# Performance work log

Measured on AMD Instinct MI355X. Metric: run time of the kernel, lower is better.

## Reference

```python
import jax, jax.numpy as jnp
import numpy as np
import math

IN_FEATURES = 256
OUT_FEATURES = 128
B, N = 4, 4096


def setup_inputs() -> dict:
    key = jax.random.key(0)
    ks = jax.random.split(key, 8)
    h = jax.random.normal(ks[0], (B, N, IN_FEATURES), dtype=jnp.float32)
    adj = jax.random.randint(ks[1], (B, N, N), 0, 2, dtype=jnp.int32)
    # Linear params (torch nn.Linear: y = x @ W.T + b)
    s = 1.0 / math.sqrt(IN_FEATURES)
    Wq = jax.random.uniform(ks[2], (OUT_FEATURES, IN_FEATURES), jnp.float32, -s, s)
    bq = jax.random.uniform(ks[3], (OUT_FEATURES,), jnp.float32, -s, s)
    Wk = jax.random.uniform(ks[4], (OUT_FEATURES, IN_FEATURES), jnp.float32, -s, s)
    bk = jax.random.uniform(ks[5], (OUT_FEATURES,), jnp.float32, -s, s)
    Wv = jax.random.uniform(ks[6], (OUT_FEATURES, IN_FEATURES), jnp.float32, -s, s)
    bv = jax.random.uniform(ks[7], (OUT_FEATURES,), jnp.float32, -s, s)
    return {"h": h, "adj": adj, "Wq": Wq, "bq": bq, "Wk": Wk, "bk": bk, "Wv": Wv, "bv": bv}


def reference(h, adj, Wq, bq, Wk, bk, Wv, bv):
    # QKV projections: [B, N, D]
    q = jnp.einsum('bnf,df->bnd', h, Wq) + bq
    k = jnp.einsum('bnf,df->bnd', h, Wk) + bk
    v = jnp.einsum('bnf,df->bnd', h, Wv) + bv
    # Dense scores [B, N, N], scaled
    scores = jnp.einsum('bnd,bmd->bnm', q, k) / math.sqrt(OUT_FEATURES)
    neg = jnp.float32(-9e15)
    scores = jnp.where(adj > 0, scores, neg)
    probs = jax.nn.softmax(scores, axis=-1)
    return jnp.einsum('bnm,bmd->bnd', probs, v)
```

## Files before the change

kernel.cpp:

```cpp
#include <hip/hip_runtime.h>
#include <stdint.h>
#include <math.h>

#define NB 4
#define NN 4096
#define NF 256
#define ND 128
#define KVB 32
#define NR (NB * NN)
#define QKVE ((size_t)NR * ND)

typedef __bf16 bf16x8 __attribute__((ext_vector_type(8)));
typedef __bf16 bf16x4v __attribute__((ext_vector_type(4)));
typedef float f32x4 __attribute__((ext_vector_type(4)));
typedef unsigned short u16x4 __attribute__((ext_vector_type(4)));

__device__ __forceinline__ unsigned short f2bf(float f) {
    union { float f; uint32_t u; } v; v.f = f;
    uint32_t r = (v.u + 0x7FFFu + ((v.u >> 16) & 1u)) >> 16;
    return (unsigned short)r;
}
__device__ __forceinline__ bf16x8 lds_read16(const unsigned short* base, int byte_off) {
    return *reinterpret_cast<const bf16x8*>(reinterpret_cast<const char*>(base) + byte_off);
}
__device__ __forceinline__ void gld_lds16(const void* g, void* l) {
    __builtin_amdgcn_global_load_lds(
        (const __attribute__((address_space(1))) void*)g,
        (__attribute__((address_space(3))) void*)l, 16, 0, 0);
}

__global__ __launch_bounds__(256) void pack_proj(
    const int* __restrict__ adj, unsigned long long* __restrict__ pm64,
    const float* __restrict__ h,
    const float* __restrict__ Wq, const float* __restrict__ bq,
    const float* __restrict__ Wk, const float* __restrict__ bk,
    const float* __restrict__ Wv, const float* __restrict__ bv,
    unsigned short* __restrict__ qo, unsigned short* __restrict__ ko,
    unsigned short* __restrict__ vs, float qscale)
{
    __shared__ unsigned short h_lds[64 * 128];
    __shared__ unsigned short w_lds[128 * 128];

    const int tid = threadIdx.x;
    const int lane = tid & 63;

    if (blockIdx.x < 1024) {
        const int w = tid >> 6;
        const size_t base = ((size_t)blockIdx.x * 4 + w) * 256;
        for (int o = 0; o < 32; ++o) {
            const size_t wb = base + o * 8;
            int v[8];
#pragma unroll
            for (int u = 0; u < 8; ++u)
                v[u] = adj[(wb + u) * 64 + lane];
            unsigned long long m[8];
#pragma unroll
            for (int u = 0; u < 8; ++u)
                m[u] = __ballot(v[u] != 0);
            if (lane == 0) {
#pragma unroll
                for (int u = 0; u < 8; u += 2) {
                    ulonglong2 st; st.x = m[u]; st.y = m[u + 1];
                    *reinterpret_cast<ulonglong2*>(pm64 + wb + u) = st;
                }
            }
        }
        return;
    }

    const int idx = blockIdx.x - 1024;
    const int proj = idx >> 8;
    const int R0 = (idx & 255) * 64;
    const int wv = tid >> 6;
    const int l15 = lane & 15;
    const int lhi = lane >> 4;

    const float* W    = proj == 0 ? Wq : (proj == 1 ? Wk : Wv);
    const float* bias = proj == 0 ? bq : (proj == 1 ? bk : bv);
    const float scale = proj == 0 ? qscale : 1.0f;

    f32x4 acc[8];
#pragma unroll
    for (int i = 0; i < 8; ++i) acc[i] = f32x4{0.f, 0.f, 0.f, 0.f};

    for (int kc = 0; kc < 2; ++kc) {
        const int c0 = kc * 128;
        __syncthreads();
#pragma unroll
        for (int p = 0; p < 8; ++p) {
            int i2 = p * 256 + tid;
            int row = i2 >> 5;
            int seg = i2 & 31;
            f32x4 hv = *reinterpret_cast<const f32x4*>(h + (size_t)(R0 + row) * NF + c0 + seg * 4);
            u16x4 hb;
            hb[0] = f2bf(hv[0]); hb[1] = f2bf(hv[1]); hb[2] = f2bf(hv[2]); hb[3] = f2bf(hv[3]);
            int byte = (row * 256 + seg * 8) ^ ((row & 7) << 4);
            *reinterpret_cast<u16x4*>(reinterpret_cast<char*>(h_lds) + byte) = hb;
        }
#pragma unroll
        for (int p = 0; p < 16; ++p) {
            int i2 = p * 256 + tid;
            int row = i2 >> 5;
            int seg = i2 & 31;
            f32x4 wv4 = *reinterpret_cast<const f32x4*>(W + (size_t)row * NF + c0 + seg * 4);
            u16x4 wb;
            wb[0] = f2bf(wv4[0]); wb[1] = f2bf(wv4[1]); wb[2] = f2bf(wv4[2]); wb[3] = f2bf(wv4[3]);
            int byte = (row * 256 + seg * 8) ^ ((row & 7) << 4);
            *reinterpret_cast<u16x4*>(reinterpret_cast<char*>(w_lds) + byte) = wb;
        }
        __syncthreads();
        const int arow = 16 * wv + l15;
#pragma unroll
        for (int ks = 0; ks < 4; ++ks) {
            int k = ks * 32 + 8 * lhi;
            bf16x8 a = lds_read16(h_lds, (arow * 256 + k * 2) ^ ((arow & 7) << 4));
#pragma unroll
            for (int cs = 0; cs < 8; ++cs) {
                int d = 16 * cs + l15;
                bf16x8 b = lds_read16(w_lds, (d * 256 + k * 2) ^ ((d & 7) << 4));
                acc[cs] = __builtin_amdgcn_mfma_f32_16x16x32_bf16(a, b, acc[cs], 0, 0, 0);
            }
        }
    }
    if (proj < 2) {
        unsigned short* out = proj == 0 ? qo : ko;
#pragma unroll
        for (int cs = 0; cs < 8; ++cs) {
            int d = 16 * cs + l15;
            float bb = bias[d];
#pragma unroll
            for (int j = 0; j < 4; ++j) {
                int row = R0 + 16 * wv + 4 * lhi + j;
                out[(size_t)row * ND + d] = f2bf((acc[cs][j] + bb) * scale);
            }
        }
    } else {
        const int bb_ = R0 >> 12;
        const int nb_ = (R0 & (NN - 1)) + 16 * wv + 4 * lhi;
        const int pt = nb_ >> 5;
        const int ch = (nb_ >> 3) & 3;
        const int mm0 = nb_ & 7;
#pragma unroll
        for (int cs = 0; cs < 8; ++cs) {
            int d = 16 * cs + l15;
            float bb = bias[d];
            u16x4 o;
#pragma unroll
            for (int j = 0; j < 4; ++j) o[j] = f2bf(acc[cs][j] + bb);
            size_t oidx = ((size_t)(bb_ * 128 + pt)) * 4096 + ch * 1024 + d * 8 + mm0;
            *reinterpret_cast<u16x4*>(vs + oidx) = o;
        }
    }
}

__global__ __launch_bounds__(256, 2) void attn(
    const unsigned short* __restrict__ Q,
    const unsigned short* __restrict__ K,
    const unsigned short* __restrict__ VS,
    const unsigned int* __restrict__ pm,
    float* __restrict__ out,
    float* __restrict__ opart1,
    float* __restrict__ ml,
    int ntl)
{
    __shared__ unsigned short stA[8192];
    __shared__ unsigned short stB[8192];
    __shared__ unsigned short p_lds[4096];

    const int tid = threadIdx.x;
    const int lane = tid & 63;
    const int w = tid >> 6;
    const int l15 = lane & 15;
    const int lhi = lane >> 4;

    const int flat = blockIdx.x;
    const int x = flat & 7;
    const int rest = flat >> 3;
    const int qt = rest & 31;
    const int s2 = rest >> 5;
    const int combo = x + 8 * s2;
    const int b = combo & 3;
    const int sp = combo >> 2;
    const int q0w = qt * 128 + w * 32;
    const size_t bN = (size_t)b * NN;
    const int ptbase = sp * ntl;

    const unsigned short* Kb = K + bN * ND;
    const unsigned short* Vbase = VS + (size_t)b * 128 * 4096;

    bf16x8 qf[2][4];
#pragma unroll
    for (int g = 0; g < 2; ++g)
#pragma unroll
        for (int ks = 0; ks < 4; ++ks)
            qf[g][ks] = *reinterpret_cast<const bf16x8*>(
                Q + (bN + q0w + g * 16 + l15) * ND + ks * 32 + 8 * lhi);

    const unsigned int* pmr0 = pm + (bN + (size_t)(q0w + l15)) * 128;
    const unsigned int* pmr1 = pm + (bN + (size_t)(q0w + 16 + l15)) * 128;

    f32x4 acc[2][8];
#pragma unroll
    for (int g = 0; g < 2; ++g)
#pragma unroll
        for (int i = 0; i < 8; ++i) acc[g][i] = f32x4{0.f, 0.f, 0.f, 0.f};
    float m_run[2] = {-INFINITY, -INFINITY};
    float l_part[2] = {0.f, 0.f};

    auto stage = [&](unsigned short* st, int pt) {
        const int m0 = pt * KVB;
#pragma unroll
        for (int i = 0; i < 4; ++i) {
            int c = w * 4 + i;
            if (c < 8) {
                int ms = c >> 2, ks = c & 3;
                const unsigned short* src = Kb
                    + (size_t)(m0 + ms * 16 + l15) * ND + ks * 32 + lhi * 8;
                gld_lds16(src, st + c * 512);
            } else {
                int vi = c - 8;
                const unsigned short* src = Vbase + (size_t)pt * 4096 + vi * 512 + lane * 8;
                gld_lds16(src, st + 4096 + vi * 512);
            }
        }
    };

    auto compute = [&](const unsigned short* st, unsigned int mw0, unsigned int mw1) {
        bf16x8 kf[2][4];
#pragma unroll
        for (int ms = 0; ms < 2; ++ms)
#pragma unroll
            for (int ks = 0; ks < 4; ++ks)
                kf[ms][ks] = lds_read16(st, (ms * 4 + ks) * 1024 + lane * 16);

        f32x4 s[2][2];
#pragma unroll
        for (int g = 0; g < 2; ++g)
#pragma unroll
            for (int ms = 0; ms < 2; ++ms) s[g][ms] = f32x4{0.f, 0.f, 0.f, 0.f};
        __builtin_amdgcn_s_setprio(1);
#pragma unroll
        for (int g = 0; g < 2; ++g)
#pragma unroll
            for (int ms = 0; ms < 2; ++ms)
#pragma unroll
                for (int ks = 0; ks < 4; ++ks)
                    s[g][ms] = __builtin_amdgcn_mfma_f32_16x16x32_bf16(
                        kf[ms][ks], qf[g][ks], s[g][ms], 0, 0, 0);
        __builtin_amdgcn_s_setprio(0);

        bf16x8 vf[8];
#pragma unroll
        for (int ds = 0; ds < 8; ++ds)
            vf[ds] = lds_read16(st + 4096, lhi * 2048 + ds * 256 + l15 * 16);

        const unsigned int mw[2] = {mw0, mw1};
        float smaxl[2];
        float dmax = -INFINITY;
#pragma unroll
        for (int g = 0; g < 2; ++g) {
            unsigned int mwg = mw[g] >> (4 * lhi);
#pragma unroll
            for (int ms = 0; ms < 2; ++ms)
#pragma unroll
                for (int r = 0; r < 4; ++r)
                    if (!((mwg >> (16 * ms + r)) & 1u)) s[g][ms][r] = -1.0e30f;
            float mx = fmaxf(fmaxf(fmaxf(s[g][0][0], s[g][0][1]), fmaxf(s[g][0][2], s[g][0][3])),
                             fmaxf(fmaxf(s[g][1][0], s[g][1][1]), fmaxf(s[g][1][2], s[g][1][3])));
            smaxl[g] = mx;
            dmax = fmaxf(dmax, mx - m_run[g]);
        }
        if (!__all(dmax <= 8.0f)) {
#pragma unroll
            for (int g = 0; g < 2; ++g) {
                float mx = smaxl[g];
                mx = fmaxf(mx, __shfl_xor(mx, 16, 64));
                mx = fmaxf(mx, __shfl_xor(mx, 32, 64));
                float mnew = fmaxf(m_run[g], mx);
                float c = exp2f(m_run[g] - mnew);
                m_run[g] = mnew;
                l_part[g] *= c;
#pragma unroll
                for (int ds = 0; ds < 8; ++ds) acc[g][ds] *= c;
            }
        }

#pragma unroll
        for (int g = 0; g < 2; ++g) {
            bf16x4v pbv[2];
#pragma unroll
            for (int ms = 0; ms < 2; ++ms)
#pragma unroll
                for (int r = 0; r < 4; ++r) {
                    float p = exp2f(s[g][ms][r] - m_run[g]);
                    __bf16 pb = (__bf16)p;
                    l_part[g] += (float)pb;
                    pbv[ms][r] = pb;
                }
            const int base = (w * 2 + g) * 1024 + l15 * 64;
#pragma unroll
            for (int ms = 0; ms < 2; ++ms)
                *reinterpret_cast<bf16x4v*>(reinterpret_cast<char*>(p_lds)
                    + base + ms * 32 + lhi * 8) = pbv[ms];
            bf16x8 pa = lds_read16(p_lds, base + lhi * 16);
            __builtin_amdgcn_s_setprio(1);
#pragma unroll
            for (int ds = 0; ds < 8; ++ds)
                acc[g][ds] = __builtin_amdgcn_mfma_f32_16x16x32_bf16(
                    vf[ds], pa, acc[g][ds], 0, 0, 0);
            __builtin_amdgcn_s_setprio(0);
        }
    };

    stage(stA, ptbase);
    __syncthreads();

    uint4 mk[2], mk2[2];
    mk[0] = *reinterpret_cast<const uint4*>(pmr0 + ptbase);
    mk[1] = *reinterpret_cast<const uint4*>(pmr1 + ptbase);
    for (int t = 0; t < ntl; t += 4) {
        int tn4 = (t + 4 < ntl) ? t + 4 : t;
        mk2[0] = *reinterpret_cast<const uint4*>(pmr0 + ptbase + tn4);
        mk2[1] = *reinterpret_cast<const uint4*>(pmr1 + ptbase + tn4);

        stage(stB, ptbase + t + 1);
        compute(stA, mk[0].x, mk[1].x);
        __syncthreads();
        stage(stA, ptbase + t + 2 < ptbase + ntl ? ptbase + t + 2 : ptbase + ntl - 1);
        compute(stB, mk[0].y, mk[1].y);
        __syncthreads();
        stage(stB, ptbase + t + 3 < ptbase + ntl ? ptbase + t + 3 : ptbase + ntl - 1);
        compute(stA, mk[0].z, mk[1].z);
        __syncthreads();
        stage(stA, ptbase + (t + 4 < ntl ? t + 4 : ntl - 1));
        compute(stB, mk[0].w, mk[1].w);
        __syncthreads();

        mk[0] = mk2[0]; mk[1] = mk2[1];
    }

#pragma unroll
    for (int g = 0; g < 2; ++g) {
        float rs = l_part[g];
        rs += __shfl_xor(rs, 16, 64);
        rs += __shfl_xor(rs, 32, 64);
        l_part[g] = rs;
    }

    float* op = (sp == 0) ? out : (opart1 + (size_t)(sp - 1) * NR * ND);
#pragma unroll
    for (int g = 0; g < 2; ++g) {
        const size_t rowbase = (bN + q0w + g * 16 + l15) * ND;
#pragma unroll
        for (int ds = 0; ds < 8; ++ds)
            *reinterpret_cast<f32x4*>(op + rowbase + 16 * ds + 4 * lhi) = acc[g][ds];
    }
    if (lhi == 0) {
#pragma unroll
        for (int g = 0; g < 2; ++g) {
            size_t gr = bN + q0w + g * 16 + l15;
            *reinterpret_cast<float2*>(ml + ((size_t)sp * NR + gr) * 2) =
                make_float2(m_run[g], l_part[g]);
        }
    }
}

__global__ __launch_bounds__(256) void merge_splits(
    float* __restrict__ out, const float* __restrict__ opart1,
    const float* __restrict__ ml, int nsplit)
{
    int idx = blockIdx.x * 256 + threadIdx.x;
    int row = idx >> 5;
    int d4 = (idx & 31) * 4;
    float mmax = ml[(size_t)row * 2];
    for (int sp = 1; sp < nsplit; ++sp)
        mmax = fmaxf(mmax, ml[((size_t)sp * NR + row) * 2]);
    f32x4 o0 = *reinterpret_cast<const f32x4*>(out + (size_t)row * ND + d4);
    float w0 = exp2f(ml[(size_t)row * 2] - mmax);
    float lsum = ml[(size_t)row * 2 + 1] * w0;
    f32x4 acc;
#pragma unroll
    for (int j = 0; j < 4; ++j) acc[j] = o0[j] * w0;
    for (int sp = 1; sp < nsplit; ++sp) {
        float m_s = ml[((size_t)sp * NR + row) * 2];
        float l_s = ml[((size_t)sp * NR + row) * 2 + 1];
        float ws_ = exp2f(m_s - mmax);
        f32x4 os = *reinterpret_cast<const f32x4*>(opart1 + ((size_t)(sp - 1) * NR + row) * ND + d4);
#pragma unroll
        for (int j = 0; j < 4; ++j) acc[j] += os[j] * ws_;
        lsum += l_s * ws_;
    }
    float inv = 1.0f / lsum;
    f32x4 r;
#pragma unroll
    for (int j = 0; j < 4; ++j) r[j] = acc[j] * inv;
    *reinterpret_cast<f32x4*>(out + (size_t)row * ND + d4) = r;
}

extern "C" void kernel_launch(void* const* d_in, const int* in_sizes, int n_in,
                              void* d_out, int out_size, void* d_ws, size_t ws_size,
                              hipStream_t stream) {
    const float* h  = (const float*)d_in[0];
    const int* adj  = (const int*)d_in[1];
    const float* Wq = (const float*)d_in[2];
    const float* bq = (const float*)d_in[3];
    const float* Wk = (const float*)d_in[4];
    const float* bk = (const float*)d_in[5];
    const float* Wv = (const float*)d_in[6];
    const float* bv = (const float*)d_in[7];
    float* out = (float*)d_out;

    unsigned short* qws  = (unsigned short*)d_ws;
    unsigned short* kws  = qws + QKVE;
    unsigned short* vsws = kws + QKVE;
    float* opart1 = (float*)(vsws + QKVE);

    const size_t pm_bytes = (size_t)NB * NN * (NN / 8);
    const size_t need4 = 3 * QKVE * 2 + 3 * QKVE * 4 + 4 * (size_t)NR * 2 * 4 + pm_bytes;
    const int nsplit = (ws_size >= need4) ? 4 : 2;
    float* mlws = opart1 + (size_t)(nsplit - 1) * NR * ND;
    unsigned int* pmws = (unsigned int*)(mlws + (size_t)nsplit * NR * 2);
    const int ntl = (NN / KVB) / nsplit;

    const float qscale = (float)(0.08838834764831845 / 0.6931471805599453);

    pack_proj<<<dim3(1024 + 768), 256, 0, stream>>>(
        adj, (unsigned long long*)pmws,
        h, Wq, bq, Wk, bk, Wv, bv, qws, kws, vsws, qscale);
    attn<<<dim3(32 * 4 * nsplit), 256, 0, stream>>>(
        qws, kws, vsws, pmws, out, opart1, mlws, ntl);
    merge_splits<<<dim3(NR * 32 / 256), 256, 0, stream>>>(out, opart1, mlws, nsplit);
}
```

Measured before the change: 152.8 us.

## Read int32 adjacency directly in attention instead of pre-packing bitmask

Removes the separate adjacency bit-packing pass from the projection kernel. The attention kernel now loads int32 adjacency values per tile straight from global memory, double-buffered alongside the K/V staging. This drops one full read of the 256MB adjacency plus the packed-mask write and re-read. In exchange the attention kernel reads 32x more mask bytes per tile inside its main loop, which may make it memory-bound.

Measured after the change: 124.6 us (median of 2 runs). -18.5%, faster.

```diff
diff --git a/kernel.cpp b/kernel.cpp
--- a/kernel.cpp
+++ b/kernel.cpp
@@ -13,6 +13,7 @@
 typedef __bf16 bf16x8 __attribute__((ext_vector_type(8)));
 typedef __bf16 bf16x4v __attribute__((ext_vector_type(4)));
 typedef float f32x4 __attribute__((ext_vector_type(4)));
+typedef int i32x4 __attribute__((ext_vector_type(4)));
 typedef unsigned short u16x4 __attribute__((ext_vector_type(4)));
 
 __device__ __forceinline__ unsigned short f2bf(float f) {
@@ -29,8 +30,7 @@
         (__attribute__((address_space(3))) void*)l, 16, 0, 0);
 }
 
-__global__ __launch_bounds__(256) void pack_proj(
-    const int* __restrict__ adj, unsigned long long* __restrict__ pm64,
+__global__ __launch_bounds__(256) void qkv_proj(
     const float* __restrict__ h,
     const float* __restrict__ Wq, const float* __restrict__ bq,
     const float* __restrict__ Wk, const float* __restrict__ bk,
@@ -43,34 +43,8 @@
 
     const int tid = threadIdx.x;
     const int lane = tid & 63;
-
-    if (blockIdx.x < 1024) {
-        const int w = tid >> 6;
-        const size_t base = ((size_t)blockIdx.x * 4 + w) * 256;
-        for (int o = 0; o < 32; ++o) {
-            const size_t wb = base + o * 8;
-            int v[8];
-#pragma unroll
-            for (int u = 0; u < 8; ++u)
-                v[u] = adj[(wb + u) * 64 + lane];
-            unsigned long long m[8];
-#pragma unroll
-            for (int u = 0; u < 8; ++u)
-                m[u] = __ballot(v[u] != 0);
-            if (lane == 0) {
-#pragma unroll
-                for (int u = 0; u < 8; u += 2) {
-                    ulonglong2 st; st.x = m[u]; st.y = m[u + 1];
-                    *reinterpret_cast<ulonglong2*>(pm64 + wb + u) = st;
-                }
-            }
-        }
-        return;
-    }
-
-    const int idx = blockIdx.x - 1024;
-    const int proj = idx >> 8;
-    const int R0 = (idx & 255) * 64;
+    const int proj = blockIdx.x >> 8;
+    const int R0 = (blockIdx.x & 255) * 64;
     const int wv = tid >> 6;
     const int l15 = lane & 15;
     const int lhi = lane >> 4;
@@ -157,7 +131,7 @@
     const unsigned short* __restrict__ Q,
     const unsigned short* __restrict__ K,
     const unsigned short* __restrict__ VS,
-    const unsigned int* __restrict__ pm,
+    const int* __restrict__ adj,
     float* __restrict__ out,
     float* __restrict__ opart1,
     float* __restrict__ ml,
@@ -187,6 +161,7 @@
 
     const unsigned short* Kb = K + bN * ND;
     const unsigned short* Vbase = VS + (size_t)b * 128 * 4096;
+    const int* adjb = adj + (size_t)b * NN * NN + (size_t)(q0w + l15) * NN + 4 * lhi;
 
     bf16x8 qf[2][4];
 #pragma unroll
@@ -195,9 +170,6 @@
         for (int ks = 0; ks < 4; ++ks)
             qf[g][ks] = *reinterpret_cast<const bf16x8*>(
                 Q + (bN + q0w + g * 16 + l15) * ND + ks * 32 + 8 * lhi);
-
-    const unsigned int* pmr0 = pm + (bN + (size_t)(q0w + l15)) * 128;
-    const unsigned int* pmr1 = pm + (bN + (size_t)(q0w + 16 + l15)) * 128;
 
     f32x4 acc[2][8];
 #pragma unroll
@@ -224,8 +196,17 @@
             }
         }
     };
-
-    auto compute = [&](const unsigned short* st, unsigned int mw0, unsigned int mw1) {
+    auto adjld = [&](i32x4 (&ma)[2][2], int pt) {
+        const int m0 = pt * KVB;
+#pragma unroll
+        for (int g = 0; g < 2; ++g)
+#pragma unroll
+            for (int ms = 0; ms < 2; ++ms)
+                ma[g][ms] = *reinterpret_cast<const i32x4*>(
+                    adjb + (size_t)(g * 16) * NN + m0 + 16 * ms);
+    };
+
+    auto compute = [&](const unsigned short* st, const i32x4 (&ma)[2][2]) {
         bf16x8 kf[2][4];
 #pragma unroll
         for (int ms = 0; ms < 2; ++ms)
@@ -254,17 +235,15 @@
         for (int ds = 0; ds < 8; ++ds)
             vf[ds] = lds_read16(st + 4096, lhi * 2048 + ds * 256 + l15 * 16);
 
-        const unsigned int mw[2] = {mw0, mw1};
         float smaxl[2];
         float dmax = -INFINITY;
 #pragma unroll
         for (int g = 0; g < 2; ++g) {
-            unsigned int mwg = mw[g] >> (4 * lhi);
 #pragma unroll
             for (int ms = 0; ms < 2; ++ms)
 #pragma unroll
                 for (int r = 0; r < 4; ++r)
-                    if (!((mwg >> (16 * ms + r)) & 1u)) s[g][ms][r] = -1.0e30f;
+                    if (ma[g][ms][r] == 0) s[g][ms][r] = -1.0e30f;
             float mx = fmaxf(fmaxf(fmaxf(s[g][0][0], s[g][0][1]), fmaxf(s[g][0][2], s[g][0][3])),
                              fmaxf(fmaxf(s[g][1][0], s[g][1][1]), fmaxf(s[g][1][2], s[g][1][3])));
             smaxl[g] = mx;
@@ -312,31 +291,21 @@
         }
     };
 
+    i32x4 maskA[2][2], maskB[2][2];
     stage(stA, ptbase);
+    adjld(maskA, ptbase);
     __syncthreads();
 
-    uint4 mk[2], mk2[2];
-    mk[0] = *reinterpret_cast<const uint4*>(pmr0 + ptbase);
-    mk[1] = *reinterpret_cast<const uint4*>(pmr1 + ptbase);
-    for (int t = 0; t < ntl; t += 4) {
-        int tn4 = (t + 4 < ntl) ? t + 4 : t;
-        mk2[0] = *reinterpret_cast<const uint4*>(pmr0 + ptbase + tn4);
-        mk2[1] = *reinterpret_cast<const uint4*>(pmr1 + ptbase + tn4);
-
+    for (int t = 0; t < ntl; t += 2) {
         stage(stB, ptbase + t + 1);
-        compute(stA, mk[0].x, mk[1].x);
+        adjld(maskB, ptbase + t + 1);
+        compute(stA, maskA);
         __syncthreads();
-        stage(stA, ptbase + t + 2 < ptbase + ntl ? ptbase + t + 2 : ptbase + ntl - 1);
-        compute(stB, mk[0].y, mk[1].y);
+        int t2 = (t + 2 < ntl) ? t + 2 : ntl - 1;
+        stage(stA, ptbase + t2);
+        adjld(maskA, ptbase + t2);
+        compute(stB, maskB);
         __syncthreads();
-        stage(stB, ptbase + t + 3 < ptbase + ntl ? ptbase + t + 3 : ptbase + ntl - 1);
-        compute(stA, mk[0].z, mk[1].z);
-        __syncthreads();
-        stage(stA, ptbase + (t + 4 < ntl ? t + 4 : ntl - 1));
-        compute(stB, mk[0].w, mk[1].w);
-        __syncthreads();
-
-        mk[0] = mk2[0]; mk[1] = mk2[1];
     }
 
 #pragma unroll
@@ -415,19 +384,16 @@
     unsigned short* vsws = kws + QKVE;
     float* opart1 = (float*)(vsws + QKVE);
 
-    const size_t pm_bytes = (size_t)NB * NN * (NN / 8);
-    const size_t need4 = 3 * QKVE * 2 + 3 * QKVE * 4 + 4 * (size_t)NR * 2 * 4 + pm_bytes;
+    const size_t need4 = 3 * QKVE * 2 + 3 * QKVE * 4 + 4 * (size_t)NR * 2 * 4;
     const int nsplit = (ws_size >= need4) ? 4 : 2;
     float* mlws = opart1 + (size_t)(nsplit - 1) * NR * ND;
-    unsigned int* pmws = (unsigned int*)(mlws + (size_t)nsplit * NR * 2);
     const int ntl = (NN / KVB) / nsplit;
 
     const float qscale = (float)(0.08838834764831845 / 0.6931471805599453);
 
-    pack_proj<<<dim3(1024 + 768), 256, 0, stream>>>(
-        adj, (unsigned long long*)pmws,
+    qkv_proj<<<dim3(768), 256, 0, stream>>>(
         h, Wq, bq, Wk, bk, Wv, bv, qws, kws, vsws, qscale);
     attn<<<dim3(32 * 4 * nsplit), 256, 0, stream>>>(
-        qws, kws, vsws, pmws, out, opart1, mlws, ntl);
+        qws, kws, vsws, adj, out, opart1, mlws, ntl);
     merge_splits<<<dim3(NR * 32 / 256), 256, 0, stream>>>(out, opart1, mlws, nsplit);
 }
```
